# Kernel tuning notes

Hardware: AMD Instinct MI355X
Metric: run time of the kernel (lower is better)

## Reference

```python
import jax, jax.numpy as jnp
import numpy as np

N_NODES = 100000
N_EDGES = 1600000
IN_F, HID_F, OUT_F = 128, 128, 64


def gcn_conv(x, edge_index, W, b):
    # x: [N, Fin]; W: [Fout, Fin] (torch Linear layout); b: [Fout]
    h = x @ W.T + b  # [N, Fout]
    src, dst = edge_index[0], edge_index[1]
    n = x.shape[0]
    # in-degree via scatter-add of ones on dst (matches torch code)
    deg = jax.ops.segment_sum(jnp.ones(src.shape[0], dtype=h.dtype), dst, num_segments=n)
    deg_inv_sqrt = jnp.where(deg > 0, deg ** -0.5, 0.0)
    w = deg_inv_sqrt[src] * deg_inv_sqrt[dst]  # edge_weight defaults to ones
    msg = w[:, None] * h[src]  # [E, Fout] gather + scale
    return jax.ops.segment_sum(msg, dst, num_segments=n)  # scatter-add aggregate


def setup_inputs() -> dict:
    key = jax.random.key(0)
    k1, k2, k3, k4 = jax.random.split(key, 4)
    x = jax.random.normal(k1, (N_NODES, IN_F), dtype=jnp.float32)
    edge_index = jax.random.randint(k2, (2, N_EDGES), 0, N_NODES, dtype=jnp.int64)
    # xavier-uniform-like weights, zero bias (torch Linear layout [out, in])
    lim1 = float(np.sqrt(6.0 / (IN_F + HID_F)))
    lim2 = float(np.sqrt(6.0 / (HID_F + OUT_F)))
    W1 = jax.random.uniform(k3, (HID_F, IN_F), jnp.float32, -lim1, lim1)
    W2 = jax.random.uniform(k4, (OUT_F, HID_F), jnp.float32, -lim2, lim2)
    b1 = jnp.zeros((HID_F,), jnp.float32)
    b2 = jnp.zeros((OUT_F,), jnp.float32)
    return {"x": x, "edge_index": edge_index, "W1": W1, "b1": b1, "W2": W2, "b2": b2}


def reference(x, edge_index, W1, b1, W2, b2):
    # layer 1 + relu (dropout is identity in eval mode)
    h = jax.nn.relu(gcn_conv(x, edge_index, W1, b1))
    # final layer, no activation
    return gcn_conv(h, edge_index, W2, b2)
```

## Files before the change

kernel.cpp:

```cpp
#include <hip/hip_runtime.h>

constexpr int FIN    = 128;
constexpr int LOG_RB = 7;
constexpr int RB     = 1 << LOG_RB;
constexpr int BMAX   = 1024;
constexpr int CAP    = 8192;
constexpr int CHUNK  = 4096;

typedef _Float16 half8 __attribute__((ext_vector_type(8)));
typedef float    f32x4 __attribute__((ext_vector_type(4)));

__global__ __launch_bounds__(1024) void init_gcur_kernel(int* __restrict__ gcur, int B) {
    int i = blockIdx.x * 1024 + threadIdx.x;
    if (i < B) gcur[i] = i * CAP;
}

__global__ __launch_bounds__(256) void bucket_scatter_kernel(
    const int* __restrict__ src, const int* __restrict__ dst,
    int* __restrict__ gcur, unsigned* __restrict__ gEdges, int E, int B)
{
    __shared__ int lhist[BMAX];
    __shared__ int lbase[BMAX];
    __shared__ int lcur[BMAX];
    const int e0 = blockIdx.x * CHUNK;
    const int e1 = min(e0 + CHUNK, E);
    for (int i = threadIdx.x; i < B; i += 256) { lhist[i] = 0; lcur[i] = 0; }
    __syncthreads();
    for (int e = e0 + threadIdx.x; e < e1; e += 256)
        atomicAdd(&lhist[dst[e] >> LOG_RB], 1);
    __syncthreads();
    for (int i = threadIdx.x; i < B; i += 256) {
        int c = lhist[i];
        if (c) lbase[i] = atomicAdd(&gcur[i], c);
    }
    __syncthreads();
    for (int e = e0 + threadIdx.x; e < e1; e += 256) {
        int d = dst[e];
        int b = d >> LOG_RB;
        int pos = lbase[b] + atomicAdd(&lcur[b], 1);
        if (pos < (b + 1) * CAP)
            gEdges[pos] = ((unsigned)src[e] << LOG_RB) | (unsigned)(d & (RB - 1));
    }
}

__global__ __launch_bounds__(256) void finalize_kernel(
    const unsigned* __restrict__ gEdges, const int* __restrict__ gcur,
    int* __restrict__ rbeg, int* __restrict__ rend, float* __restrict__ dis,
    int* __restrict__ esrc, int N)
{
    __shared__ int h[RB];
    __shared__ int excl[RB];
    __shared__ int cur[RB];
    const int b = blockIdx.x;
    const int base = b * CAP;
    int cnt = gcur[b] - base;
    if (cnt > CAP) cnt = CAP;
    const int node0 = b << LOG_RB;
    if (threadIdx.x < RB) h[threadIdx.x] = 0;
    __syncthreads();
    for (int i = threadIdx.x; i < cnt; i += 256)
        atomicAdd(&h[gEdges[base + i] & (RB - 1)], 1);
    __syncthreads();
    if (threadIdx.x < RB) excl[threadIdx.x] = h[threadIdx.x];
    __syncthreads();
    for (int off = 1; off < RB; off <<= 1) {
        int u = 0;
        if (threadIdx.x < RB && threadIdx.x >= off) u = excl[threadIdx.x - off];
        __syncthreads();
        if (threadIdx.x < RB) excl[threadIdx.x] += u;
        __syncthreads();
    }
    if (threadIdx.x < RB) {
        int c  = h[threadIdx.x];
        int ex = excl[threadIdx.x] - c;
        cur[threadIdx.x] = ex;
        int node = node0 + threadIdx.x;
        if (node < N) {
            rbeg[node] = base + ex;
            rend[node] = base + ex + c;
            dis[node]  = c > 0 ? rsqrtf((float)c) : 0.0f;
        }
    }
    __syncthreads();
    for (int i = threadIdx.x; i < cnt; i += 256) {
        unsigned p = gEdges[base + i];
        int dl = (int)(p & (RB - 1));
        int pos = base + atomicAdd(&cur[dl], 1);
        esrc[pos] = (int)(p >> LOG_RB);
    }
}

__global__ __launch_bounds__(256) void linear1_kernel(
    const float* __restrict__ X, const float* __restrict__ W,
    const float* __restrict__ Bv, const float* __restrict__ dis,
    _Float16* __restrict__ Y, int N)
{
    __shared__ __align__(16) _Float16 xs[64 * 128];
    const int tid  = threadIdx.x;
    const int wave = tid >> 6;
    const int lane = tid & 63;
    const int l15  = lane & 15;
    const int lhi  = lane >> 4;

    half8 wf[2][4];
    float bias[2];
    #pragma unroll
    for (int c = 0; c < 2; ++c) {
        int f = (wave * 2 + c) * 16 + l15;
        #pragma unroll
        for (int ks = 0; ks < 4; ++ks) {
            const float* wp = &W[f * 128 + ks * 32 + lhi * 8];
            float4 u0 = *(const float4*)wp;
            float4 u1 = *(const float4*)(wp + 4);
            half8 hh;
            hh[0] = (_Float16)u0.x; hh[1] = (_Float16)u0.y;
            hh[2] = (_Float16)u0.z; hh[3] = (_Float16)u0.w;
            hh[4] = (_Float16)u1.x; hh[5] = (_Float16)u1.y;
            hh[6] = (_Float16)u1.z; hh[7] = (_Float16)u1.w;
            wf[c][ks] = hh;
        }
        bias[c] = Bv[f];
    }

    const int nchunks = (N + 63) / 64;
    for (int ch = blockIdx.x; ch < nchunks; ch += gridDim.x) {
        const int n0 = ch * 64;
        __syncthreads();
        #pragma unroll
        for (int p = 0; p < 4; ++p) {
            int ci  = p * 256 + tid;
            int row = ci >> 4, c = ci & 15;
            int n   = n0 + row;
            int nc  = n < N ? n : N - 1;
            const float* xp = &X[(size_t)nc * 128 + c * 8];
            float4 u0 = *(const float4*)xp;
            float4 u1 = *(const float4*)(xp + 4);
            half8 hh;
            hh[0] = (_Float16)u0.x; hh[1] = (_Float16)u0.y;
            hh[2] = (_Float16)u0.z; hh[3] = (_Float16)u0.w;
            hh[4] = (_Float16)u1.x; hh[5] = (_Float16)u1.y;
            hh[6] = (_Float16)u1.z; hh[7] = (_Float16)u1.w;
            *(half8*)&xs[row * 128 + (c ^ (row & 7)) * 8] = hh;
        }
        __syncthreads();

        f32x4 acc[4][2];
        #pragma unroll
        for (int mt = 0; mt < 4; ++mt)
            #pragma unroll
            for (int c = 0; c < 2; ++c) {
                acc[mt][c][0] = bias[c]; acc[mt][c][1] = bias[c];
                acc[mt][c][2] = bias[c]; acc[mt][c][3] = bias[c];
            }

        #pragma unroll
        for (int mt = 0; mt < 4; ++mt) {
            int row = mt * 16 + l15;
            #pragma unroll
            for (int ks = 0; ks < 4; ++ks) {
                int c  = ks * 4 + lhi;
                half8 a = *(const half8*)&xs[row * 128 + (c ^ (row & 7)) * 8];
                #pragma unroll
                for (int c2 = 0; c2 < 2; ++c2)
                    acc[mt][c2] = __builtin_amdgcn_mfma_f32_16x16x32_f16(
                        a, wf[c2][ks], acc[mt][c2], 0, 0, 0);
            }
        }
        __syncthreads();
        #pragma unroll
        for (int mt = 0; mt < 4; ++mt)
            #pragma unroll
            for (int r = 0; r < 4; ++r) {
                int row = mt * 16 + lhi * 4 + r;
                int n   = n0 + row;
                int nc  = n < N ? n : N - 1;
                float dv = dis[nc];
                #pragma unroll
                for (int c2 = 0; c2 < 2; ++c2) {
                    int col = (wave * 2 + c2) * 16 + l15;
                    xs[row * 128 + col] = (_Float16)(dv * acc[mt][c2][r]);
                }
            }
        __syncthreads();
        #pragma unroll
        for (int p = 0; p < 4; ++p) {
            int ci  = p * 256 + tid;
            int row = ci >> 4, c = ci & 15;
            int n   = n0 + row;
            if (n < N)
                *(half8*)&Y[(size_t)n * 128 + c * 8] = *(const half8*)&xs[row * 128 + c * 8];
        }
    }
}

__global__ __launch_bounds__(256) void aggregate128h_kernel(
    const _Float16* __restrict__ H, const int* __restrict__ rbeg,
    const int* __restrict__ rend, const int* __restrict__ esrc,
    const float* __restrict__ dis, _Float16* __restrict__ OUT, int N)
{
    const int lane = threadIdx.x & 15;
    const int d = blockIdx.x * 16 + (threadIdx.x >> 4);
    if (d >= N) return;
    const int beg = rbeg[d], end = rend[d];
    float acc[4][8];
    #pragma unroll
    for (int u = 0; u < 4; ++u)
        #pragma unroll
        for (int j = 0; j < 8; ++j) acc[u][j] = 0.0f;
    int e = beg;
    for (; e + 4 <= end; e += 4) {
        int s0 = esrc[e], s1 = esrc[e+1], s2 = esrc[e+2], s3 = esrc[e+3];
        half8 v0 = *(const half8*)&H[(size_t)s0 * 128 + lane * 8];
        half8 v1 = *(const half8*)&H[(size_t)s1 * 128 + lane * 8];
        half8 v2 = *(const half8*)&H[(size_t)s2 * 128 + lane * 8];
        half8 v3 = *(const half8*)&H[(size_t)s3 * 128 + lane * 8];
        #pragma unroll
        for (int j = 0; j < 8; ++j) {
            acc[0][j] += (float)v0[j]; acc[1][j] += (float)v1[j];
            acc[2][j] += (float)v2[j]; acc[3][j] += (float)v3[j];
        }
    }
    for (; e < end; ++e) {
        int s0 = esrc[e];
        half8 v0 = *(const half8*)&H[(size_t)s0 * 128 + lane * 8];
        #pragma unroll
        for (int j = 0; j < 8; ++j) acc[0][j] += (float)v0[j];
    }
    float w = dis[d];
    half8 o;
    #pragma unroll
    for (int j = 0; j < 8; ++j) {
        float t = w * ((acc[0][j] + acc[1][j]) + (acc[2][j] + acc[3][j]));
        o[j] = (_Float16)fmaxf(t, 0.0f);
    }
    *(half8*)&OUT[(size_t)d * 128 + lane * 8] = o;
}

__global__ __launch_bounds__(256) void lin2_kernel(
    const _Float16* __restrict__ Xh, const float* __restrict__ W,
    const float* __restrict__ Bv, const float* __restrict__ dis,
    _Float16* __restrict__ Y, int N)
{
    __shared__ __align__(16) _Float16 xs[64 * 128];
    const int tid  = threadIdx.x;
    const int wave = tid >> 6;
    const int lane = tid & 63;
    const int l15  = lane & 15;
    const int lhi  = lane >> 4;

    half8 wf[4];
    float bias;
    {
        int f = wave * 16 + l15;
        #pragma unroll
        for (int ks = 0; ks < 4; ++ks) {
            const float* wp = &W[f * 128 + ks * 32 + lhi * 8];
            float4 u0 = *(const float4*)wp;
            float4 u1 = *(const float4*)(wp + 4);
            half8 hh;
            hh[0] = (_Float16)u0.x; hh[1] = (_Float16)u0.y;
            hh[2] = (_Float16)u0.z; hh[3] = (_Float16)u0.w;
            hh[4] = (_Float16)u1.x; hh[5] = (_Float16)u1.y;
            hh[6] = (_Float16)u1.z; hh[7] = (_Float16)u1.w;
            wf[ks] = hh;
        }
        bias = Bv[f];
    }

    const int nchunks = (N + 63) / 64;
    for (int ch = blockIdx.x; ch < nchunks; ch += gridDim.x) {
        const int n0 = ch * 64;
        __syncthreads();
        #pragma unroll
        for (int p = 0; p < 4; ++p) {
            int ci  = p * 256 + tid;
            int row = ci >> 4, c = ci & 15;
            int n   = n0 + row;
            int nc  = n < N ? n : N - 1;
            half8 hh = *(const half8*)&Xh[(size_t)nc * 128 + c * 8];
            *(half8*)&xs[row * 128 + (c ^ (row & 7)) * 8] = hh;
        }
        __syncthreads();

        f32x4 acc[4];
        #pragma unroll
        for (int mt = 0; mt < 4; ++mt) {
            acc[mt][0] = bias; acc[mt][1] = bias;
            acc[mt][2] = bias; acc[mt][3] = bias;
        }
        #pragma unroll
        for (int mt = 0; mt < 4; ++mt) {
            int row = mt * 16 + l15;
            #pragma unroll
            for (int ks = 0; ks < 4; ++ks) {
                int c  = ks * 4 + lhi;
                half8 a = *(const half8*)&xs[row * 128 + (c ^ (row & 7)) * 8];
                acc[mt] = __builtin_amdgcn_mfma_f32_16x16x32_f16(a, wf[ks], acc[mt], 0, 0, 0);
            }
        }
        __syncthreads();
        #pragma unroll
        for (int mt = 0; mt < 4; ++mt)
            #pragma unroll
            for (int r = 0; r < 4; ++r) {
                int row = mt * 16 + lhi * 4 + r;
                int n   = n0 + row;
                int nc  = n < N ? n : N - 1;
                float dv = dis[nc];
                xs[row * 64 + wave * 16 + l15] = (_Float16)(dv * acc[mt][r]);
            }
        __syncthreads();
        #pragma unroll
        for (int p = 0; p < 2; ++p) {
            int ci  = p * 256 + tid;
            int row = ci >> 3, c = ci & 7;
            int n   = n0 + row;
            if (n < N)
                *(half8*)&Y[(size_t)n * 64 + c * 8] = *(const half8*)&xs[row * 64 + c * 8];
        }
    }
}

__global__ __launch_bounds__(256) void aggregate64h_kernel(
    const _Float16* __restrict__ H, const int* __restrict__ rbeg,
    const int* __restrict__ rend, const int* __restrict__ esrc,
    const float* __restrict__ dis, float* __restrict__ OUT, int N)
{
    const int lane = threadIdx.x & 7;
    const int d = blockIdx.x * 32 + (threadIdx.x >> 3);
    if (d >= N) return;
    const int beg = rbeg[d], end = rend[d];
    float a0[8] = {0,0,0,0,0,0,0,0}, a1[8] = {0,0,0,0,0,0,0,0};
    int e = beg;
    for (; e + 4 <= end; e += 4) {
        int s0 = esrc[e], s1 = esrc[e+1], s2 = esrc[e+2], s3 = esrc[e+3];
        half8 v0 = *(const half8*)&H[(size_t)s0 * 64 + lane * 8];
        half8 v1 = *(const half8*)&H[(size_t)s1 * 64 + lane * 8];
        half8 v2 = *(const half8*)&H[(size_t)s2 * 64 + lane * 8];
        half8 v3 = *(const half8*)&H[(size_t)s3 * 64 + lane * 8];
        #pragma unroll
        for (int j = 0; j < 8; ++j) {
            a0[j] += (float)v0[j]; a1[j] += (float)v1[j];
            a0[j] += (float)v2[j]; a1[j] += (float)v3[j];
        }
    }
    for (; e < end; ++e) {
        int s0 = esrc[e];
        half8 v0 = *(const half8*)&H[(size_t)s0 * 64 + lane * 8];
        #pragma unroll
        for (int j = 0; j < 8; ++j) a0[j] += (float)v0[j];
    }
    float w = dis[d];
    float4 o0, o1;
    o0.x = w * (a0[0] + a1[0]); o0.y = w * (a0[1] + a1[1]);
    o0.z = w * (a0[2] + a1[2]); o0.w = w * (a0[3] + a1[3]);
    o1.x = w * (a0[4] + a1[4]); o1.y = w * (a0[5] + a1[5]);
    o1.z = w * (a0[6] + a1[6]); o1.w = w * (a0[7] + a1[7]);
    float* p = &OUT[(size_t)d * 64 + lane * 8];
    *(float4*)p = o0;
    *(float4*)(p + 4) = o1;
}

template <int FOUT, bool RELU_IN>
__global__ __launch_bounds__(256) void linear_kernel(
    const float* __restrict__ X, const float* __restrict__ W,
    const float* __restrict__ Bv, float* __restrict__ Y, int N)
{
    constexpr int TX = FOUT / 4;
    constexpr int TY = 256 / TX;
    constexpr int NB = 4 * TY;
    constexpr int QMASK = TX - 1;
    __shared__ float ws[FIN * FOUT];
    __shared__ float xs[NB * FIN];
    const int tid = threadIdx.x;
    const int tx  = tid % TX;
    const int ty  = tid / TX;
    for (int i = tid; i < FOUT * FIN; i += 256) {
        int f = i >> 7;
        int k = i & (FIN - 1);
        int q = f >> 2, r = f & 3;
        int qq = q ^ (k & QMASK);
        ws[k * FOUT + qq * 4 + r] = W[i];
    }
    const float4 bv = *(const float4*)&Bv[tx * 4];
    const int nchunks = (N + NB - 1) / NB;
    for (int c = blockIdx.x; c < nchunks; c += gridDim.x) {
        const int n0 = c * NB;
        __syncthreads();
        constexpr int V4 = FIN / 4;
        for (int i4 = tid; i4 < NB * V4; i4 += 256) {
            int row = i4 / V4, c4 = i4 % V4;
            int n = n0 + row;
            int nc = n < N ? n : N - 1;
            float4 v = *(const float4*)&X[(long long)nc * FIN + c4 * 4];
            if (RELU_IN) {
                v.x = fmaxf(v.x, 0.0f); v.y = fmaxf(v.y, 0.0f);
                v.z = fmaxf(v.z, 0.0f); v.w = fmaxf(v.w, 0.0f);
            }
            *(float4*)&xs[row * FIN + c4 * 4] = v;
        }
        __syncthreads();
        float acc[4][4];
        #pragma unroll
        for (int j = 0; j < 4; ++j) {
            acc[j][0] = bv.x; acc[j][1] = bv.y; acc[j][2] = bv.z; acc[j][3] = bv.w;
        }
        #pragma unroll 2
        for (int k = 0; k < FIN; k += 4) {
            float w[4][4];
            #pragma unroll
            for (int kk = 0; kk < 4; ++kk) {
                int kr = k + kk;
                float4 t = *(const float4*)&ws[kr * FOUT + ((tx ^ (kr & QMASK)) << 2)];
                w[kk][0] = t.x; w[kk][1] = t.y; w[kk][2] = t.z; w[kk][3] = t.w;
            }
            float xr[4][4];
            #pragma unroll
            for (int j = 0; j < 4; ++j) {
                float4 t = *(const float4*)&xs[(ty * 4 + j) * FIN + k];
                xr[j][0] = t.x; xr[j][1] = t.y; xr[j][2] = t.z; xr[j][3] = t.w;
            }
            #pragma unroll
            for (int j = 0; j < 4; ++j)
                #pragma unroll
                for (int kk = 0; kk < 4; ++kk) {
                    acc[j][0] = fmaf(xr[j][kk], w[kk][0], acc[j][0]);
                    acc[j][1] = fmaf(xr[j][kk], w[kk][1], acc[j][1]);
                    acc[j][2] = fmaf(xr[j][kk], w[kk][2], acc[j][2]);
                    acc[j][3] = fmaf(xr[j][kk], w[kk][3], acc[j][3]);
                }
        }
        #pragma unroll
        for (int j = 0; j < 4; ++j) {
            int n = n0 + ty * 4 + j;
            if (n < N) {
                float4 o;
                o.x = acc[j][0]; o.y = acc[j][1]; o.z = acc[j][2]; o.w = acc[j][3];
                *(float4*)&Y[(long long)n * FOUT + tx * 4] = o;
            }
        }
    }
}

template <int LOGF>
__global__ __launch_bounds__(256) void scatter_kernel(
    const float* __restrict__ H, const int* __restrict__ src,
    const int* __restrict__ dst, const float* __restrict__ dis,
    float* __restrict__ OUT, int E)
{
    constexpr int F = 1 << LOGF;
    const long long total  = (long long)E << LOGF;
    const long long stride = (long long)gridDim.x * blockDim.x;
    for (long long i = (long long)blockIdx.x * blockDim.x + threadIdx.x;
         i < total; i += stride) {
        int e = (int)(i >> LOGF);
        int f = (int)i & (F - 1);
        int s = src[e];
        int d = dst[e];
        float w = dis[s] * dis[d];
        atomicAdd(&OUT[d * F + f], w * H[s * F + f]);
    }
}

__global__ __launch_bounds__(256) void dis_inplace_kernel(float* __restrict__ deg, int N) {
    int i = blockIdx.x * 256 + threadIdx.x;
    if (i < N) {
        float d = deg[i];
        deg[i] = d > 0.0f ? rsqrtf(d) : 0.0f;
    }
}

__global__ __launch_bounds__(256) void deg_kernel_f(const int* __restrict__ dst,
                                                    float* __restrict__ deg, int E) {
    int stride = gridDim.x * 256;
    for (int i = blockIdx.x * 256 + threadIdx.x; i < E; i += stride)
        atomicAdd(&deg[dst[i]], 1.0f);
}

static inline size_t align512(size_t x) { return (x + 511) & ~(size_t)511; }

extern "C" void kernel_launch(void* const* d_in, const int* in_sizes, int n_in,
                              void* d_out, int out_size, void* d_ws, size_t ws_size,
                              hipStream_t stream)
{
    const float* x  = (const float*)d_in[0];
    const int*   ei = (const int*)d_in[1];
    const float* W1 = (const float*)d_in[2];
    const float* b1 = (const float*)d_in[3];
    const float* W2 = (const float*)d_in[4];
    const float* b2 = (const float*)d_in[5];

    const int N = in_sizes[0] / FIN;
    const int E = in_sizes[1] / 2;
    const int* src = ei;
    const int* dst = ei + E;
    float* out = (float*)d_out;
    char* wsb = (char*)d_ws;

    const int B = (N + RB - 1) / RB;

    size_t hreg = (size_t)N * 128 * 2;
    size_t areg = (size_t)B * CAP * 4;
    size_t h1sz = hreg > areg ? hreg : areg;
    size_t o = 0;
    int*      gcur  = (int*)(wsb + o);      o = align512(o + (size_t)BMAX * 4);
    int*      rbeg  = (int*)(wsb + o);      o = align512(o + (size_t)N * 4);
    int*      rendp = (int*)(wsb + o);      o = align512(o + (size_t)N * 4);
    float*    dis   = (float*)(wsb + o);    o = align512(o + (size_t)N * 4);
    int*      esrcA = (int*)(wsb + o);      o = align512(o + areg);
    _Float16* h1    = (_Float16*)(wsb + o); o = align512(o + h1sz);
    _Float16* agg1  = (_Float16*)(wsb + o); o = align512(o + (size_t)N * 128 * 2);
    _Float16* h2    = (_Float16*)(wsb + o); o = align512(o + (size_t)N * 64 * 2);
    size_t need = o;
    unsigned* gEdges = (unsigned*)h1;

    if (ws_size >= need && B <= BMAX) {
        init_gcur_kernel<<<(B + 1023) / 1024, 1024, 0, stream>>>(gcur, B);
        bucket_scatter_kernel<<<(E + CHUNK - 1) / CHUNK, 256, 0, stream>>>(
            src, dst, gcur, gEdges, E, B);
        finalize_kernel<<<B, 256, 0, stream>>>(gEdges, gcur, rbeg, rendp, dis, esrcA, N);

        linear1_kernel<<<512, 256, 0, stream>>>(x, W1, b1, dis, h1, N);
        aggregate128h_kernel<<<(N + 15) / 16, 256, 0, stream>>>(h1, rbeg, rendp,
                                                                esrcA, dis, agg1, N);
        lin2_kernel<<<512, 256, 0, stream>>>(agg1, W2, b2, dis, h2, N);
        aggregate64h_kernel<<<(N + 31) / 32, 256, 0, stream>>>(h2, rbeg, rendp,
                                                               esrcA, dis, out, N);
    } else {
        float* deg  = (float*)wsb;
        size_t off  = align512((size_t)N * 4);
        float* fh1  = (float*)(wsb + off);
        float* fagg = fh1 + (size_t)N * FIN;
        float* fh2  = fh1;

        hipMemsetAsync(deg,  0, (size_t)N * 4, stream);
        hipMemsetAsync(fagg, 0, (size_t)N * FIN * 4, stream);
        hipMemsetAsync(out,  0, (size_t)N * 64 * 4, stream);

        deg_kernel_f<<<2048, 256, 0, stream>>>(dst, deg, E);
        dis_inplace_kernel<<<(N + 255) / 256, 256, 0, stream>>>(deg, N);

        linear_kernel<128, false><<<512, 256, 0, stream>>>(x, W1, b1, fh1, N);
        scatter_kernel<7><<<8192, 256, 0, stream>>>(fh1, src, dst, deg, fagg, E);
        linear_kernel<64, true><<<512, 256, 0, stream>>>(fagg, W2, b2, fh2, N);
        scatter_kernel<6><<<8192, 256, 0, stream>>>(fh2, src, dst, deg, out, E);
    }
}
```

Baseline: 175.9 us.

## Prefetch edge indices in aggregation, stage bucket edges in LDS, retune bucket sizes

Both aggregation kernels now software-pipeline the source-index loads: the next group of four esrc entries is loaded while the current four feature rows are gathered, shortening the dependent load chain. The 64-wide aggregation also moves from two accumulators to four. finalize_kernel keeps bucket edges in shared memory, so gEdges is read from global memory once instead of twice. Bucket capacity drops to 4096 and the scatter chunk grows to 16384, which means fewer scatter blocks and less scratch space. The trade-off is a higher risk of bucket overflow, and edges beyond capacity are silently dropped.

```diff
diff --git a/kernel.cpp b/kernel.cpp
--- a/kernel.cpp
+++ b/kernel.cpp
@@ -4,8 +4,8 @@
 constexpr int LOG_RB = 7;
 constexpr int RB     = 1 << LOG_RB;
 constexpr int BMAX   = 1024;
-constexpr int CAP    = 8192;
-constexpr int CHUNK  = 4096;
+constexpr int CAP    = 4096;
+constexpr int CHUNK  = 16384;
 
 typedef _Float16 half8 __attribute__((ext_vector_type(8)));
 typedef float    f32x4 __attribute__((ext_vector_type(4)));
@@ -51,6 +51,7 @@
     __shared__ int h[RB];
     __shared__ int excl[RB];
     __shared__ int cur[RB];
+    __shared__ unsigned sedge[CAP];
     const int b = blockIdx.x;
     const int base = b * CAP;
     int cnt = gcur[b] - base;
@@ -58,8 +59,11 @@
     const int node0 = b << LOG_RB;
     if (threadIdx.x < RB) h[threadIdx.x] = 0;
     __syncthreads();
-    for (int i = threadIdx.x; i < cnt; i += 256)
-        atomicAdd(&h[gEdges[base + i] & (RB - 1)], 1);
+    for (int i = threadIdx.x; i < cnt; i += 256) {
+        unsigned p = gEdges[base + i];
+        sedge[i] = p;
+        atomicAdd(&h[p & (RB - 1)], 1);
+    }
     __syncthreads();
     if (threadIdx.x < RB) excl[threadIdx.x] = h[threadIdx.x];
     __syncthreads();
@@ -83,7 +87,7 @@
     }
     __syncthreads();
     for (int i = threadIdx.x; i < cnt; i += 256) {
-        unsigned p = gEdges[base + i];
+        unsigned p = sedge[i];
         int dl = (int)(p & (RB - 1));
         int pos = base + atomicAdd(&cur[dl], 1);
         esrc[pos] = (int)(p >> LOG_RB);
@@ -207,18 +211,37 @@
     for (int u = 0; u < 4; ++u)
         #pragma unroll
         for (int j = 0; j < 8; ++j) acc[u][j] = 0.0f;
+
+    const int n4 = (end - beg) >> 2;
     int e = beg;
-    for (; e + 4 <= end; e += 4) {
+    if (n4 > 0) {
         int s0 = esrc[e], s1 = esrc[e+1], s2 = esrc[e+2], s3 = esrc[e+3];
-        half8 v0 = *(const half8*)&H[(size_t)s0 * 128 + lane * 8];
-        half8 v1 = *(const half8*)&H[(size_t)s1 * 128 + lane * 8];
-        half8 v2 = *(const half8*)&H[(size_t)s2 * 128 + lane * 8];
-        half8 v3 = *(const half8*)&H[(size_t)s3 * 128 + lane * 8];
-        #pragma unroll
-        for (int j = 0; j < 8; ++j) {
-            acc[0][j] += (float)v0[j]; acc[1][j] += (float)v1[j];
-            acc[2][j] += (float)v2[j]; acc[3][j] += (float)v3[j];
-        }
+        for (int q = 1; q < n4; ++q) {
+            const int b2 = beg + q * 4;
+            int t0 = esrc[b2], t1 = esrc[b2+1], t2 = esrc[b2+2], t3 = esrc[b2+3];
+            half8 v0 = *(const half8*)&H[(size_t)s0 * 128 + lane * 8];
+            half8 v1 = *(const half8*)&H[(size_t)s1 * 128 + lane * 8];
+            half8 v2 = *(const half8*)&H[(size_t)s2 * 128 + lane * 8];
+            half8 v3 = *(const half8*)&H[(size_t)s3 * 128 + lane * 8];
+            #pragma unroll
+            for (int j = 0; j < 8; ++j) {
+                acc[0][j] += (float)v0[j]; acc[1][j] += (float)v1[j];
+                acc[2][j] += (float)v2[j]; acc[3][j] += (float)v3[j];
+            }
+            s0 = t0; s1 = t1; s2 = t2; s3 = t3;
+        }
+        {
+            half8 v0 = *(const half8*)&H[(size_t)s0 * 128 + lane * 8];
+            half8 v1 = *(const half8*)&H[(size_t)s1 * 128 + lane * 8];
+            half8 v2 = *(const half8*)&H[(size_t)s2 * 128 + lane * 8];
+            half8 v3 = *(const half8*)&H[(size_t)s3 * 128 + lane * 8];
+            #pragma unroll
+            for (int j = 0; j < 8; ++j) {
+                acc[0][j] += (float)v0[j]; acc[1][j] += (float)v1[j];
+                acc[2][j] += (float)v2[j]; acc[3][j] += (float)v3[j];
+            }
+        }
+        e = beg + n4 * 4;
     }
     for (; e < end; ++e) {
         int s0 = esrc[e];
@@ -330,32 +353,59 @@
     const int d = blockIdx.x * 32 + (threadIdx.x >> 3);
     if (d >= N) return;
     const int beg = rbeg[d], end = rend[d];
-    float a0[8] = {0,0,0,0,0,0,0,0}, a1[8] = {0,0,0,0,0,0,0,0};
+    float acc[4][8];
+    #pragma unroll
+    for (int u = 0; u < 4; ++u)
+        #pragma unroll
+        for (int j = 0; j < 8; ++j) acc[u][j] = 0.0f;
+
+    const int n4 = (end - beg) >> 2;
     int e = beg;
-    for (; e + 4 <= end; e += 4) {
+    if (n4 > 0) {
         int s0 = esrc[e], s1 = esrc[e+1], s2 = esrc[e+2], s3 = esrc[e+3];
-        half8 v0 = *(const half8*)&H[(size_t)s0 * 64 + lane * 8];
-        half8 v1 = *(const half8*)&H[(size_t)s1 * 64 + lane * 8];
-        half8 v2 = *(const half8*)&H[(size_t)s2 * 64 + lane * 8];
-        half8 v3 = *(const half8*)&H[(size_t)s3 * 64 + lane * 8];
-        #pragma unroll
-        for (int j = 0; j < 8; ++j) {
-            a0[j] += (float)v0[j]; a1[j] += (float)v1[j];
-            a0[j] += (float)v2[j]; a1[j] += (float)v3[j];
-        }
+        for (int q = 1; q < n4; ++q) {
+            const int b2 = beg + q * 4;
+            int t0 = esrc[b2], t1 = esrc[b2+1], t2 = esrc[b2+2], t3 = esrc[b2+3];
+            half8 v0 = *(const half8*)&H[(size_t)s0 * 64 + lane * 8];
+            half8 v1 = *(const half8*)&H[(size_t)s1 * 64 + lane * 8];
+            half8 v2 = *(const half8*)&H[(size_t)s2 * 64 + lane * 8];
+            half8 v3 = *(const half8*)&H[(size_t)s3 * 64 + lane * 8];
+            #pragma unroll
+            for (int j = 0; j < 8; ++j) {
+                acc[0][j] += (float)v0[j]; acc[1][j] += (float)v1[j];
+                acc[2][j] += (float)v2[j]; acc[3][j] += (float)v3[j];
+            }
+            s0 = t0; s1 = t1; s2 = t2; s3 = t3;
+        }
+        {
+            half8 v0 = *(const half8*)&H[(size_t)s0 * 64 + lane * 8];
+            half8 v1 = *(const half8*)&H[(size_t)s1 * 64 + lane * 8];
+            half8 v2 = *(const half8*)&H[(size_t)s2 * 64 + lane * 8];
+            half8 v3 = *(const half8*)&H[(size_t)s3 * 64 + lane * 8];
+            #pragma unroll
+            for (int j = 0; j < 8; ++j) {
+                acc[0][j] += (float)v0[j]; acc[1][j] += (float)v1[j];
+                acc[2][j] += (float)v2[j]; acc[3][j] += (float)v3[j];
+            }
+        }
+        e = beg + n4 * 4;
     }
     for (; e < end; ++e) {
         int s0 = esrc[e];
         half8 v0 = *(const half8*)&H[(size_t)s0 * 64 + lane * 8];
         #pragma unroll
-        for (int j = 0; j < 8; ++j) a0[j] += (float)v0[j];
+        for (int j = 0; j < 8; ++j) acc[0][j] += (float)v0[j];
     }
     float w = dis[d];
     float4 o0, o1;
-    o0.x = w * (a0[0] + a1[0]); o0.y = w * (a0[1] + a1[1]);
-    o0.z = w * (a0[2] + a1[2]); o0.w = w * (a0[3] + a1[3]);
-    o1.x = w * (a0[4] + a1[4]); o1.y = w * (a0[5] + a1[5]);
-    o1.z = w * (a0[6] + a1[6]); o1.w = w * (a0[7] + a1[7]);
+    o0.x = w * ((acc[0][0] + acc[1][0]) + (acc[2][0] + acc[3][0]));
+    o0.y = w * ((acc[0][1] + acc[1][1]) + (acc[2][1] + acc[3][1]));
+    o0.z = w * ((acc[0][2] + acc[1][2]) + (acc[2][2] + acc[3][2]));
+    o0.w = w * ((acc[0][3] + acc[1][3]) + (acc[2][3] + acc[3][3]));
+    o1.x = w * ((acc[0][4] + acc[1][4]) + (acc[2][4] + acc[3][4]));
+    o1.y = w * ((acc[0][5] + acc[1][5]) + (acc[2][5] + acc[3][5]));
+    o1.z = w * ((acc[0][6] + acc[1][6]) + (acc[2][6] + acc[3][6]));
+    o1.w = w * ((acc[0][7] + acc[1][7]) + (acc[2][7] + acc[3][7]));
     float* p = &OUT[(size_t)d * 64 + lane * 8];
     *(float4*)p = o0;
     *(float4*)(p + 4) = o1;
```

After: 202.8 us. 1.15x slower.
